# Optimization experiments

Measured on AMD Instinct MI355X. Metric: run time of the kernel, lower is better.

## Reference

```python
import jax, jax.numpy as jnp
import numpy as np

N_HEADS = 16
DIM = 1024
HEAD_DIM = DIM // N_HEADS

def setup_inputs() -> dict:
    key = jax.random.key(0)
    ks = jax.random.split(key, 5)
    x = jax.random.normal(ks[0], (4, 2048, DIM), dtype=jnp.float32)
    W_attn = jax.random.normal(ks[1], (DIM, 3 * DIM), dtype=jnp.float32) / np.sqrt(DIM)
    b_attn = jnp.zeros((3 * DIM,), dtype=jnp.float32)
    W_proj = jax.random.normal(ks[2], (DIM, DIM), dtype=jnp.float32) / np.sqrt(DIM)
    b_proj = jnp.zeros((DIM,), dtype=jnp.float32)
    return {"x": x, "W_attn": W_attn, "b_attn": b_attn, "W_proj": W_proj, "b_proj": b_proj}

def reference(x, W_attn, b_attn, W_proj, b_proj):
    B, S, D = x.shape
    qkv = x @ W_attn + b_attn                      # [B,S,3D]
    q, k, v = jnp.split(qkv, 3, axis=2)
    def heads(t):
        return t.reshape(B, S, N_HEADS, HEAD_DIM).transpose(0, 2, 1, 3)  # [B,H,S,hd]
    qh, kh, vh = heads(q), heads(k), heads(v)
    scale = 1.0 / np.sqrt(HEAD_DIM).astype(np.float32)
    scores = jnp.einsum('bhqd,bhkd->bhqk', qh, kh) * scale  # [B,H,S,S]
    causal = jnp.tril(jnp.ones((S, S), dtype=bool))
    scores = jnp.where(causal, scores, -jnp.inf)
    probs = jax.nn.softmax(scores, axis=-1)
    ctx = jnp.einsum('bhqk,bhkd->bhqd', probs, vh)           # [B,H,S,hd]
    ctx = ctx.transpose(0, 2, 1, 3).reshape(B, S, D)
    return ctx @ W_proj + b_proj
```

## Files before the change

kernel.cpp:

```cpp
#include <hip/hip_runtime.h>
#include <hip/hip_bf16.h>
#include <stdint.h>

typedef __attribute__((ext_vector_type(4))) float  f32x4a;
typedef __attribute__((ext_vector_type(8))) short  bf16x8s;
typedef __attribute__((ext_vector_type(8))) unsigned short u16x8;

#define QSCALE 0.18033688011112042f

static __device__ __forceinline__ unsigned short f2bf(float f) {
    union { float f; uint32_t u; } v; v.f = f;
    uint32_t u = v.u;
    return (unsigned short)((u + 0x7FFFu + ((u >> 16) & 1u)) >> 16);
}

static __device__ __forceinline__ unsigned int pack2bf(float lo, float hi) {
    __hip_bfloat162 t = __float22bfloat162_rn(make_float2(lo, hi));
    union { __hip_bfloat162 b; unsigned int u; } c; c.b = t;
    return c.u;
}

static __device__ __forceinline__ float exp2a(float x) {
    float r;
    asm("v_exp_f32 %0, %1" : "=v"(r) : "v"(x));
    return r;
}

#define GLL(src, dst)                                                          \
    __builtin_amdgcn_global_load_lds(                                          \
        (const __attribute__((address_space(1))) void*)(src),                  \
        (__attribute__((address_space(3))) void*)(dst), 16, 0, 0)

__global__ __launch_bounds__(256) void k_cvt_bf16(const float* __restrict__ in,
                                                  unsigned short* __restrict__ out, int n8) {
    int i = blockIdx.x * blockDim.x + threadIdx.x;
    if (i >= n8) return;
    const float4* p = (const float4*)(in + (size_t)i * 8);
    float4 a = p[0], b = p[1];
    u16x8 o;
    o[0] = f2bf(a.x); o[1] = f2bf(a.y); o[2] = f2bf(a.z); o[3] = f2bf(a.w);
    o[4] = f2bf(b.x); o[5] = f2bf(b.y); o[6] = f2bf(b.z); o[7] = f2bf(b.w);
    *(u16x8*)(out + (size_t)i * 8) = o;
}

__global__ __launch_bounds__(256) void k_scale_bias(const float* __restrict__ b,
                                                    float* __restrict__ out,
                                                    int n, int nscale, float sc) {
    int i = blockIdx.x * blockDim.x + threadIdx.x;
    if (i >= n) return;
    out[i] = b[i] * (i < nscale ? sc : 1.0f);
}

__global__ __launch_bounds__(256) void k_transpose_w(const float* __restrict__ W,
                                                     unsigned short* __restrict__ Wt,
                                                     int K, int N, float sc, int nscale) {
    __shared__ float tile[64][68];
    int bx = blockIdx.x;
    int ntn = N >> 6;
    int kt = bx / ntn, nt = bx % ntn;
    int t = threadIdx.x;
    int r0 = t >> 4;
    int c4 = (t & 15) << 2;
    for (int i = 0; i < 4; ++i) {
        int k = r0 + i * 16;
        float4 v = *(const float4*)(W + (size_t)(kt * 64 + k) * N + nt * 64 + c4);
        tile[k][c4 + 0] = v.x; tile[k][c4 + 1] = v.y;
        tile[k][c4 + 2] = v.z; tile[k][c4 + 3] = v.w;
    }
    __syncthreads();
    int nl = t >> 2;
    int kc = (t & 3) << 4;
    float s = (nt * 64 + nl < nscale) ? sc : 1.0f;
    unsigned short* dst = Wt + (size_t)(nt * 64 + nl) * K + kt * 64 + kc;
    u16x8 o0, o1;
    for (int i = 0; i < 8; ++i) o0[i] = f2bf(tile[kc + i][nl] * s);
    for (int i = 0; i < 8; ++i) o1[i] = f2bf(tile[kc + 8 + i][nl] * s);
    *(u16x8*)dst = o0;
    *(u16x8*)(dst + 8) = o1;
}

template<int OUT_BF16, int VW>
__global__ __launch_bounds__(512, 4) void k_gemm2b(const unsigned short* __restrict__ A,
                                                   const unsigned short* __restrict__ Bt,
                                                   const float* __restrict__ bias,
                                                   void* __restrict__ Cout,
                                                   unsigned short* __restrict__ vt,
                                                   int M, int N, int K, int ntn) {
    __shared__ __align__(16) unsigned short S[3][12288];
    unsigned short* Sf = &S[0][0];

    int nwg = gridDim.x;
    int bid = blockIdx.x;
    int wg = (bid & 7) * (nwg >> 3) + (bid >> 3);
    int mt = wg / ntn, nt = wg % ntn;
    size_t m0 = (size_t)mt * 128, n0 = (size_t)nt * 256;

    int tid = threadIdx.x;
    int w = tid >> 6, lane = tid & 63;
    int wm = w >> 2, wn = w & 3;
    int l15 = lane & 15, l4 = lane >> 4;

    int srow = tid >> 2;
    int sch = (tid & 3) ^ ((srow >> 1) & 3);
    const unsigned short* Asrc = A  + (m0 + srow) * (size_t)K + sch * 8;
    const unsigned short* Bsrc = Bt + (n0 + srow) * (size_t)K + sch * 8;

#define STG(bufoff, kt)                                                                   \
    do {                                                                                  \
        GLL(Asrc + (size_t)(kt) * 32,                    Sf + (bufoff) + tid * 8);        \
        GLL(Bsrc + (size_t)(kt) * 32,                    Sf + (bufoff) + 4096 + tid * 8); \
        GLL(Bsrc + (size_t)(kt) * 32 + (size_t)128 * K,  Sf + (bufoff) + 8192 + tid * 8); \
    } while (0)

    int ck = (l4 ^ ((l15 >> 1) & 3)) * 8;
    int aoff = (wm * 64 + l15) * 32 + ck;
    int boff = 4096 + (wn * 64 + l15) * 32 + ck;

    f32x4a acc[4][4] = {};

#define BAR() __builtin_amdgcn_s_barrier()

    int NT = K >> 5;

    STG(0, 0);
    STG(12288, 1);
    asm volatile("s_waitcnt vmcnt(3)" ::: "memory");
    __builtin_amdgcn_sched_barrier(0);
    BAR();

    int cb = 0;
    for (int t = 0; t < NT; ++t) {
        int sb = cb + 24576; if (sb >= 36864) sb -= 36864;
        bool more = (t + 2) < NT;
        if (more) STG(sb, t + 2);
        bf16x8s af[4], bf[4];
        #pragma unroll
        for (int q = 0; q < 4; ++q) af[q] = *(const bf16x8s*)(Sf + cb + aoff + q * 512);
        #pragma unroll
        for (int q = 0; q < 4; ++q) bf[q] = *(const bf16x8s*)(Sf + cb + boff + q * 512);
        __builtin_amdgcn_s_setprio(1);
        #pragma unroll
        for (int mf = 0; mf < 4; ++mf)
            #pragma unroll
            for (int nf = 0; nf < 4; ++nf)
                acc[mf][nf] = __builtin_amdgcn_mfma_f32_16x16x32_bf16(af[mf], bf[nf],
                                                                      acc[mf][nf], 0, 0, 0);
        __builtin_amdgcn_s_setprio(0);
        if (more) { asm volatile("s_waitcnt vmcnt(3)" ::: "memory"); }
        else      { asm volatile("s_waitcnt vmcnt(0)" ::: "memory"); }
        __builtin_amdgcn_sched_barrier(0);
        BAR();
        cb += 12288; if (cb >= 36864) cb = 0;
    }

    if (VW && nt >= 8) {
        int b = (int)(m0 >> 11);
        int sb_ = ((int)m0 & 2047) + wm * 64;
        #pragma unroll
        for (int nf = 0; nf < 4; ++nf) {
            int vc = ((int)n0 - 2048) + wn * 64 + nf * 16 + l15;
            int h = vc >> 6, d = vc & 63;
            float bv = bias[2048 + vc];
            unsigned short* vrow = vt + ((size_t)(b * 16 + h) * 64 + d) * 2048;
            #pragma unroll
            for (int mf = 0; mf < 4; ++mf) {
                int s = sb_ + mf * 16 + l4 * 4;
                uint2 pv = make_uint2(pack2bf(acc[mf][nf][0] + bv, acc[mf][nf][1] + bv),
                                      pack2bf(acc[mf][nf][2] + bv, acc[mf][nf][3] + bv));
                *(uint2*)(vrow + s) = pv;
            }
        }
    } else {
        #pragma unroll
        for (int nf = 0; nf < 4; ++nf) {
            int col = (int)n0 + wn * 64 + nf * 16 + l15;
            float bv = bias[col];
            #pragma unroll
            for (int mf = 0; mf < 4; ++mf) {
                int rbase = (int)m0 + wm * 64 + mf * 16 + l4 * 4;
                #pragma unroll
                for (int rr = 0; rr < 4; ++rr) {
                    float v = acc[mf][nf][rr] + bv;
                    if (OUT_BF16)
                        ((unsigned short*)Cout)[(size_t)(rbase + rr) * N + col] = f2bf(v);
                    else
                        ((float*)Cout)[(size_t)(rbase + rr) * N + col] = v;
                }
            }
        }
    }
#undef STG
#undef BAR
}

__global__ __launch_bounds__(256, 2) void k_attn(const unsigned short* __restrict__ qkv,
                                                 const unsigned short* __restrict__ vt,
                                                 unsigned short* __restrict__ ctx) {
    __shared__ unsigned short Ks[3][4096];
    __shared__ unsigned short Vs[3][4096];
    __shared__ unsigned short Pb[4][2048];
    int bx = blockIdx.x;
    int bh = bx & 63;
    int pr = bx >> 6;
    int b = bh >> 4, hd = bh & 15;
    int tid = threadIdx.x;
    int w = tid >> 6, lane = tid & 63;
    int l15 = lane & 15, l4 = lane >> 4;

    const unsigned short* Qb  = qkv + (size_t)b * 2048 * 3072 + hd * 64;
    const unsigned short* Kb  = Qb + 1024;
    const unsigned short* Vtb = vt + (size_t)bh * 64 * 2048;

    int kr0 = tid >> 3, kc0 = tid & 7;
    int kr1 = (tid + 256) >> 3, kc1 = tid & 7;
    const unsigned short* Ksr0 = Kb  + (size_t)kr0 * 3072 + ((kc0 ^ (kr0 & 7)) << 3);
    const unsigned short* Ksr1 = Kb  + (size_t)kr1 * 3072 + ((kc1 ^ (kr1 & 7)) << 3);
    const unsigned short* Vsr0 = Vtb + (size_t)kr0 * 2048 + ((kc0 ^ (kr0 & 7)) << 3);
    const unsigned short* Vsr1 = Vtb + (size_t)kr1 * 2048 + ((kc1 ^ (kr1 & 7)) << 3);
    unsigned short* pbw = &Pb[w][0];

    int psw  = l15 & 7;
    int ph   = (l4 & 1) * 4;
    int pc0  = ((0 + (l4 >> 1)) ^ psw) * 8;
    int pc1  = ((2 + (l4 >> 1)) ^ psw) * 8;
    int pc2  = ((4 + (l4 >> 1)) ^ psw) * 8;
    int pc3  = ((6 + (l4 >> 1)) ^ psw) * 8;
    int pr0  = ((0 + l4) ^ psw) * 8;
    int pr1  = ((4 + l4) ^ psw) * 8;
    int prow0 = l15 * 64;
    int prow1 = (l15 + 16) * 64;

    bf16x8s onesf;
    #pragma unroll
    for (int i = 0; i < 8; ++i) onesf[i] = (short)0x3F80;

#define STAGE(buf, kv0s)                                                                        \
    do {                                                                                        \
        size_t ko_ = (size_t)(kv0s) * 3072;                                                     \
        GLL(Ksr0 + ko_,     &Ks[buf][w * 512]);                                                 \
        GLL(Ksr1 + ko_,     &Ks[buf][2048 + w * 512]);                                          \
        GLL(Vsr0 + (kv0s),  &Vs[buf][w * 512]);                                                 \
        GLL(Vsr1 + (kv0s),  &Vs[buf][2048 + w * 512]);                                          \
    } while (0)

    for (int half = 0; half < 2; ++half) {
        int j = half ? (15 - pr) : pr;
        int q0 = j * 128 + w * 32;
        int qa0 = q0 + l15, qa1 = q0 + 16 + l15;
        bf16x8s qf[2][2];
        {
            const unsigned short* p0 = Qb + (size_t)(q0 + l15) * 3072 + l4 * 8;
            qf[0][0] = *(const bf16x8s*)p0;
            qf[0][1] = *(const bf16x8s*)(p0 + 32);
            const unsigned short* p1 = p0 + (size_t)16 * 3072;
            qf[1][0] = *(const bf16x8s*)p1;
            qf[1][1] = *(const bf16x8s*)(p1 + 32);
        }
        f32x4a o[2][4] = {};
        f32x4a lsum[2] = {};
        const int NSTEPS = 2 * j + 2;

        STAGE(0, 0);
        STAGE(1, 64);
        asm volatile("s_waitcnt vmcnt(4)" ::: "memory");
        __builtin_amdgcn_sched_barrier(0);
        __builtin_amdgcn_s_barrier();

        int s = 0, cur = 0;
        while (true) {
            int kv0 = s << 6;
            bool stg = (s + 2 < NSTEPS);
            int sb = cur + 2; if (sb >= 3) sb -= 3;
            if (stg) STAGE(sb, kv0 + 128);

            if (kv0 <= q0 + 31) {
                const unsigned short* Kbuf = Ks[cur];
                const unsigned short* Vbuf = Vs[cur];

                bf16x8s vf[2][4];
                #pragma unroll
                for (int g = 0; g < 2; ++g)
                    #pragma unroll
                    for (int nf = 0; nf < 4; ++nf) {
                        int rv = nf * 16 + l15;
                        vf[g][nf] = *(const bf16x8s*)(Vbuf + rv * 64 + (((g * 4 + l4) ^ (rv & 7)) << 3));
                    }

                f32x4a z[2][4];
                __builtin_amdgcn_s_setprio(1);
                #pragma unroll
                for (int f = 0; f < 4; ++f) {
                    int rk = f * 16 + l15;
                    bf16x8s ka = *(const bf16x8s*)(Kbuf + rk * 64 + ((l4 ^ psw) << 3));
                    bf16x8s kb = *(const bf16x8s*)(Kbuf + rk * 64 + (((4 + l4) ^ psw) << 3));
                    #pragma unroll
                    for (int g = 0; g < 2; ++g) {
                        f32x4a zz = {0.f, 0.f, 0.f, 0.f};
                        zz = __builtin_amdgcn_mfma_f32_16x16x32_bf16(ka, qf[g][0], zz, 0, 0, 0);
                        zz = __builtin_amdgcn_mfma_f32_16x16x32_bf16(kb, qf[g][1], zz, 0, 0, 0);
                        z[g][f] = zz;
                    }
                }
                __builtin_amdgcn_s_setprio(0);

                if (kv0 + 63 > q0) {
                    #pragma unroll
                    for (int f = 0; f < 4; ++f)
                        #pragma unroll
                        for (int r = 0; r < 4; ++r) {
                            int kvp = kv0 + f * 16 + l4 * 4 + r;
                            if (kvp > qa0) z[0][f][r] = -1e30f;
                            if (kvp > qa1) z[1][f][r] = -1e30f;
                        }
                }

                f32x4a p4[2][4];
                #pragma unroll
                for (int g = 0; g < 2; ++g)
                    #pragma unroll
                    for (int f = 0; f < 4; ++f)
                        #pragma unroll
                        for (int r = 0; r < 4; ++r)
                            p4[g][f][r] = exp2a(z[g][f][r]);

                unsigned int pk[2][8];
                #pragma unroll
                for (int g = 0; g < 2; ++g)
                    #pragma unroll
                    for (int f = 0; f < 4; ++f) {
                        pk[g][2 * f]     = pack2bf(p4[g][f][0], p4[g][f][1]);
                        pk[g][2 * f + 1] = pack2bf(p4[g][f][2], p4[g][f][3]);
                    }

                *(uint2*)(pbw + prow0 + pc0 + ph) = make_uint2(pk[0][0], pk[0][1]);
                *(uint2*)(pbw + prow0 + pc1 + ph) = make_uint2(pk[0][2], pk[0][3]);
                *(uint2*)(pbw + prow0 + pc2 + ph) = make_uint2(pk[0][4], pk[0][5]);
                *(uint2*)(pbw + prow0 + pc3 + ph) = make_uint2(pk[0][6], pk[0][7]);
                *(uint2*)(pbw + prow1 + pc0 + ph) = make_uint2(pk[1][0], pk[1][1]);
                *(uint2*)(pbw + prow1 + pc1 + ph) = make_uint2(pk[1][2], pk[1][3]);
                *(uint2*)(pbw + prow1 + pc2 + ph) = make_uint2(pk[1][4], pk[1][5]);
                *(uint2*)(pbw + prow1 + pc3 + ph) = make_uint2(pk[1][6], pk[1][7]);
                asm volatile("" ::: "memory");
                bf16x8s pa[2][2];
                pa[0][0] = *(const bf16x8s*)(pbw + prow0 + pr0);
                pa[0][1] = *(const bf16x8s*)(pbw + prow0 + pr1);
                pa[1][0] = *(const bf16x8s*)(pbw + prow1 + pr0);
                pa[1][1] = *(const bf16x8s*)(pbw + prow1 + pr1);
                asm volatile("" ::: "memory");

                __builtin_amdgcn_s_setprio(1);
                #pragma unroll
                for (int hh = 0; hh < 2; ++hh)
                    #pragma unroll
                    for (int g = 0; g < 2; ++g) {
                        #pragma unroll
                        for (int nf = 0; nf < 4; ++nf)
                            o[g][nf] = __builtin_amdgcn_mfma_f32_16x16x32_bf16(
                                pa[g][hh], vf[hh][nf], o[g][nf], 0, 0, 0);
                        lsum[g] = __builtin_amdgcn_mfma_f32_16x16x32_bf16(
                            pa[g][hh], onesf, lsum[g], 0, 0, 0);
                    }
                __builtin_amdgcn_s_setprio(0);
            }

            ++s;
            if (s == NSTEPS) break;
            if (stg) { asm volatile("s_waitcnt vmcnt(4)" ::: "memory"); }
            else     { asm volatile("s_waitcnt vmcnt(0)" ::: "memory"); }
            __builtin_amdgcn_sched_barrier(0);
            __builtin_amdgcn_s_barrier();
            cur = cur + 1; if (cur == 3) cur = 0;
        }
        __syncthreads();

        float linv0[4], linv1[4];
        #pragma unroll
        for (int r = 0; r < 4; ++r) {
            linv0[r] = 1.0f / lsum[0][r];
            linv1[r] = 1.0f / lsum[1][r];
        }
        #pragma unroll
        for (int nf = 0; nf < 4; ++nf) {
            int col = hd * 64 + nf * 16 + l15;
            #pragma unroll
            for (int r = 0; r < 4; ++r) {
                int row0 = q0 + l4 * 4 + r;
                ctx[((size_t)b * 2048 + row0) * 1024 + col]      = f2bf(o[0][nf][r] * linv0[r]);
                ctx[((size_t)b * 2048 + row0 + 16) * 1024 + col] = f2bf(o[1][nf][r] * linv1[r]);
            }
        }
    }
#undef STAGE
}

extern "C" void kernel_launch(void* const* d_in, const int* in_sizes, int n_in,
                              void* d_out, int out_size, void* d_ws, size_t ws_size,
                              hipStream_t stream) {
    const float* x      = (const float*)d_in[0];
    const float* W_attn = (const float*)d_in[1];
    const float* b_attn = (const float*)d_in[2];
    const float* W_proj = (const float*)d_in[3];
    const float* b_proj = (const float*)d_in[4];

    char* ws = (char*)d_ws;
    unsigned short* xb  = (unsigned short*)ws; ws += (size_t)8192 * 1024 * 2;
    unsigned short* wta = (unsigned short*)ws; ws += (size_t)3072 * 1024 * 2;
    unsigned short* wtp = (unsigned short*)ws; ws += (size_t)1024 * 1024 * 2;
    unsigned short* qkv = (unsigned short*)ws; ws += (size_t)8192 * 3072 * 2;
    unsigned short* vt  = (unsigned short*)ws; ws += (size_t)64 * 64 * 2048 * 2;
    unsigned short* ctx = (unsigned short*)ws; ws += (size_t)8192 * 1024 * 2;
    float*          sbias = (float*)ws;

    k_cvt_bf16<<<4096, 256, 0, stream>>>(x, xb, 8192 * 1024 / 8);
    k_transpose_w<<<16 * 48, 256, 0, stream>>>(W_attn, wta, 1024, 3072, QSCALE, 1024);
    k_transpose_w<<<16 * 16, 256, 0, stream>>>(W_proj, wtp, 1024, 1024, 1.0f, 0);
    k_scale_bias<<<12, 256, 0, stream>>>(b_attn, sbias, 3072, 1024, QSCALE);
    k_gemm2b<1, 1><<<768, 512, 0, stream>>>(xb, wta, sbias, (void*)qkv, vt, 8192, 3072, 1024, 12);
    k_attn<<<512, 256, 0, stream>>>(qkv, vt, ctx);
    k_gemm2b<0, 0><<<256, 512, 0, stream>>>(ctx, wtp, b_proj, d_out, nullptr, 8192, 1024, 1024, 4);
}
```

Before: 155.7 us.

## Use double-buffered 128-key tiles in attention and drop GEMM setprio

The attention kernel's K/V staging moves from a triple-buffered ring of 64-key tiles to double-buffered 128-key tiles. Each tile is processed as two 64-key halves, which halves the number of barrier and waitcnt points per query tile. The cost is that the kernel now waits for all loads (vmcnt 0) each step, so less load is kept in flight, and shared memory use grows. Separately, the s_setprio raise around the MFMA block in the GEMM kernel is removed.

```diff
diff --git a/kernel.cpp b/kernel.cpp
--- a/kernel.cpp
+++ b/kernel.cpp
@@ -138,14 +138,12 @@
         for (int q = 0; q < 4; ++q) af[q] = *(const bf16x8s*)(Sf + cb + aoff + q * 512);
         #pragma unroll
         for (int q = 0; q < 4; ++q) bf[q] = *(const bf16x8s*)(Sf + cb + boff + q * 512);
-        __builtin_amdgcn_s_setprio(1);
         #pragma unroll
         for (int mf = 0; mf < 4; ++mf)
             #pragma unroll
             for (int nf = 0; nf < 4; ++nf)
                 acc[mf][nf] = __builtin_amdgcn_mfma_f32_16x16x32_bf16(af[mf], bf[nf],
                                                                       acc[mf][nf], 0, 0, 0);
-        __builtin_amdgcn_s_setprio(0);
         if (more) { asm volatile("s_waitcnt vmcnt(3)" ::: "memory"); }
         else      { asm volatile("s_waitcnt vmcnt(0)" ::: "memory"); }
         __builtin_amdgcn_sched_barrier(0);
@@ -196,8 +194,8 @@
 __global__ __launch_bounds__(256, 2) void k_attn(const unsigned short* __restrict__ qkv,
                                                  const unsigned short* __restrict__ vt,
                                                  unsigned short* __restrict__ ctx) {
-    __shared__ unsigned short Ks[3][4096];
-    __shared__ unsigned short Vs[3][4096];
+    __shared__ unsigned short Ks[2][8192];
+    __shared__ unsigned short Vs[2][8192];
     __shared__ unsigned short Pb[4][2048];
     int bx = blockIdx.x;
     int bh = bx & 63;
@@ -211,12 +209,10 @@
     const unsigned short* Kb  = Qb + 1024;
     const unsigned short* Vtb = vt + (size_t)bh * 64 * 2048;
 
-    int kr0 = tid >> 3, kc0 = tid & 7;
-    int kr1 = (tid + 256) >> 3, kc1 = tid & 7;
-    const unsigned short* Ksr0 = Kb  + (size_t)kr0 * 3072 + ((kc0 ^ (kr0 & 7)) << 3);
-    const unsigned short* Ksr1 = Kb  + (size_t)kr1 * 3072 + ((kc1 ^ (kr1 & 7)) << 3);
-    const unsigned short* Vsr0 = Vtb + (size_t)kr0 * 2048 + ((kc0 ^ (kr0 & 7)) << 3);
-    const unsigned short* Vsr1 = Vtb + (size_t)kr1 * 2048 + ((kc1 ^ (kr1 & 7)) << 3);
+    int kr = tid >> 3, kc = tid & 7;
+    const unsigned short* Ksr = Kb + (size_t)kr * 3072 + ((kc ^ (kr & 7)) << 3);
+    int vr = tid >> 4, vc = tid & 15;
+    const unsigned short* Vsr = Vtb + (size_t)vr * 2048 + ((vc ^ (vr & 7)) << 3);
     unsigned short* pbw = &Pb[w][0];
 
     int psw  = l15 & 7;
@@ -234,13 +230,16 @@
     #pragma unroll
     for (int i = 0; i < 8; ++i) onesf[i] = (short)0x3F80;
 
-#define STAGE(buf, kv0s)                                                                        \
-    do {                                                                                        \
-        size_t ko_ = (size_t)(kv0s) * 3072;                                                     \
-        GLL(Ksr0 + ko_,     &Ks[buf][w * 512]);                                                 \
-        GLL(Ksr1 + ko_,     &Ks[buf][2048 + w * 512]);                                          \
-        GLL(Vsr0 + (kv0s),  &Vs[buf][w * 512]);                                                 \
-        GLL(Vsr1 + (kv0s),  &Vs[buf][2048 + w * 512]);                                          \
+#define STAGE(buf, kv0s)                                                                 \
+    do {                                                                                 \
+        _Pragma("unroll")                                                                \
+        for (int i_ = 0; i_ < 4; ++i_)                                                   \
+            GLL(Ksr + (size_t)((kv0s) + 32 * i_) * 3072,                                 \
+                &Ks[buf][i_ * 2048 + w * 512]);                                          \
+        _Pragma("unroll")                                                                \
+        for (int i_ = 0; i_ < 4; ++i_)                                                   \
+            GLL(Vsr + (size_t)(16 * i_) * 2048 + (kv0s),                                 \
+                &Vs[buf][i_ * 2048 + w * 512]);                                          \
     } while (0)
 
     for (int half = 0; half < 2; ++half) {
@@ -258,24 +257,24 @@
         }
         f32x4a o[2][4] = {};
         f32x4a lsum[2] = {};
-        const int NSTEPS = 2 * j + 2;
+        const int NT128 = j + 1;
 
         STAGE(0, 0);
-        STAGE(1, 64);
-        asm volatile("s_waitcnt vmcnt(4)" ::: "memory");
+        asm volatile("s_waitcnt vmcnt(0)" ::: "memory");
         __builtin_amdgcn_sched_barrier(0);
         __builtin_amdgcn_s_barrier();
 
-        int s = 0, cur = 0;
-        while (true) {
-            int kv0 = s << 6;
-            bool stg = (s + 2 < NSTEPS);
-            int sb = cur + 2; if (sb >= 3) sb -= 3;
-            if (stg) STAGE(sb, kv0 + 128);
-
-            if (kv0 <= q0 + 31) {
-                const unsigned short* Kbuf = Ks[cur];
-                const unsigned short* Vbuf = Vs[cur];
+        for (int t = 0; t < NT128; ++t) {
+            int cur = t & 1;
+            if (t + 1 < NT128) STAGE(cur ^ 1, (t + 1) * 128);
+
+            const unsigned short* Kbuf = Ks[cur];
+            const unsigned short* Vbuf = Vs[cur];
+
+            #pragma unroll
+            for (int hh2 = 0; hh2 < 2; ++hh2) {
+                int kvh = t * 128 + hh2 * 64;
+                if (kvh > q0 + 31) continue;
 
                 bf16x8s vf[2][4];
                 #pragma unroll
@@ -283,14 +282,15 @@
                     #pragma unroll
                     for (int nf = 0; nf < 4; ++nf) {
                         int rv = nf * 16 + l15;
-                        vf[g][nf] = *(const bf16x8s*)(Vbuf + rv * 64 + (((g * 4 + l4) ^ (rv & 7)) << 3));
+                        int c  = hh2 * 8 + g * 4 + l4;
+                        vf[g][nf] = *(const bf16x8s*)(Vbuf + rv * 128 + ((c ^ (rv & 7)) << 3));
                     }
 
                 f32x4a z[2][4];
                 __builtin_amdgcn_s_setprio(1);
                 #pragma unroll
                 for (int f = 0; f < 4; ++f) {
-                    int rk = f * 16 + l15;
+                    int rk = hh2 * 64 + f * 16 + l15;
                     bf16x8s ka = *(const bf16x8s*)(Kbuf + rk * 64 + ((l4 ^ psw) << 3));
                     bf16x8s kb = *(const bf16x8s*)(Kbuf + rk * 64 + (((4 + l4) ^ psw) << 3));
                     #pragma unroll
@@ -303,12 +303,12 @@
                 }
                 __builtin_amdgcn_s_setprio(0);
 
-                if (kv0 + 63 > q0) {
+                if (kvh + 63 > q0) {
                     #pragma unroll
                     for (int f = 0; f < 4; ++f)
                         #pragma unroll
                         for (int r = 0; r < 4; ++r) {
-                            int kvp = kv0 + f * 16 + l4 * 4 + r;
+                            int kvp = kvh + f * 16 + l4 * 4 + r;
                             if (kvp > qa0) z[0][f][r] = -1e30f;
                             if (kvp > qa1) z[1][f][r] = -1e30f;
                         }
@@ -363,13 +363,9 @@
                 __builtin_amdgcn_s_setprio(0);
             }
 
-            ++s;
-            if (s == NSTEPS) break;
-            if (stg) { asm volatile("s_waitcnt vmcnt(4)" ::: "memory"); }
-            else     { asm volatile("s_waitcnt vmcnt(0)" ::: "memory"); }
+            asm volatile("s_waitcnt vmcnt(0)" ::: "memory");
             __builtin_amdgcn_sched_barrier(0);
             __builtin_amdgcn_s_barrier();
-            cur = cur + 1; if (cur == 3) cur = 0;
         }
         __syncthreads();
 
```

Result: no change. 154.8 us (-0.6%).
